# Performance work log

Hardware: AMD Instinct MI355X
Metric: run time of the kernel (lower is better)

The kernel has to match this reference:

```python
import jax, jax.numpy as jnp
import numpy as np

B, F, C = 16384, 256, 256


def setup_inputs() -> dict:
    key = jax.random.key(0)
    ks = jax.random.split(key, 10)
    return {
        "x_t": jax.random.normal(ks[0], (B, F), dtype=jnp.float32),
        "n_t": jax.random.normal(ks[1], (B, C), dtype=jnp.float32),
        "d_t": jax.random.uniform(ks[2], (B, C), dtype=jnp.float32),
        "h_t": jax.random.normal(ks[3], (B, C), dtype=jnp.float32),
        "a_max_t": jax.random.normal(ks[4], (B, C), dtype=jnp.float32),
        "Wu": jax.random.normal(ks[5], (C, F), dtype=jnp.float32) * 0.06,
        "bu": jnp.zeros((C,), dtype=jnp.float32),
        "Wg": jax.random.normal(ks[6], (C, F + C), dtype=jnp.float32) * 0.05,
        "bg": jnp.zeros((C,), dtype=jnp.float32),
        "Wa": jax.random.normal(ks[7], (C, F + C), dtype=jnp.float32) * 0.05,
        "Wd": jax.random.normal(ks[8], (C, F + C), dtype=jnp.float32) * 0.05,
    }


def reference(x_t, n_t, d_t, h_t, a_max_t, Wu, bu, Wg, bg, Wa, Wd):
    # xh_join = cat([x_t, h_t], dim=1) -> [B, F+C]
    xh = jnp.concatenate([x_t, h_t], axis=1)
    u_t = x_t @ Wu.T + bu                      # [B, C]
    g_t = xh @ Wg.T + bg                       # [B, C]
    a_t = xh @ Wa.T                            # [B, C] (no bias)
    z_t = u_t * jnp.tanh(g_t)
    # decay branch (self.decay is an nn.Linear -> always truthy in original)
    decay = jax.nn.sigmoid(xh @ Wd.T)
    e_neg = jnp.exp(-decay)
    a_decay = a_max_t * e_neg
    a_newmax = jnp.maximum(a_decay, a_t)
    exp_diff = jnp.exp(a_max_t - a_newmax)
    exp_scaled = jnp.exp(a_t - a_newmax)
    n_new = n_t * e_neg * exp_diff + z_t * exp_scaled
    d_new = d_t * e_neg * exp_diff + exp_scaled
    h_new = jnp.tanh(n_new / d_new)
    return (n_new, d_new, h_new, a_newmax)
```

## Files before the change

### kernel.cpp

```cpp
#include <hip/hip_runtime.h>
#include <stdint.h>

typedef _Float16 f16x8 __attribute__((ext_vector_type(8)));
typedef __fp16 fp16x2 __attribute__((ext_vector_type(2)));
typedef float f32x4 __attribute__((ext_vector_type(4)));

#define BC (16384 * 256)

__device__ __forceinline__ f16x8 cvt8(f32x4 a, f32x4 b) {
  fp16x2 p0 = __builtin_amdgcn_cvt_pkrtz(a[0], a[1]);
  fp16x2 p1 = __builtin_amdgcn_cvt_pkrtz(a[2], a[3]);
  fp16x2 p2 = __builtin_amdgcn_cvt_pkrtz(b[0], b[1]);
  fp16x2 p3 = __builtin_amdgcn_cvt_pkrtz(b[2], b[3]);
  f16x8 o;
  o[0] = (_Float16)p0[0]; o[1] = (_Float16)p0[1];
  o[2] = (_Float16)p1[0]; o[3] = (_Float16)p1[1];
  o[4] = (_Float16)p2[0]; o[5] = (_Float16)p2[1];
  o[6] = (_Float16)p3[0]; o[7] = (_Float16)p3[1];
  return o;
}

__device__ __forceinline__ float tanh_fast(float v) {
  float a = fminf(fabsf(v), 18.f);
  float t = __expf(2.f * a);
  float r = (t - 1.f) * __builtin_amdgcn_rcpf(t + 1.f);
  return copysignf(r, v);
}

__global__ __launch_bounds__(256) void pack_w(const float* __restrict__ Wu,
                                              const float* __restrict__ Wg,
                                              const float* __restrict__ Wa,
                                              const float* __restrict__ Wd,
                                              _Float16* __restrict__ wsB) {
  int t = blockIdx.x * 256 + threadIdx.x;
  int slot = t & 7;
  int kt = (t >> 3) & 7;
  int row = (t >> 6) & 127;
  int cb = t >> 13;
  int strip = (row >> 4) & 3;
  int wn = row >> 6;
  int t16 = row & 15;
  int c = cb * 32 + wn * 16 + t16;
  int k0 = kt * 64 + (slot ^ (row & 7)) * 8;
  float v[8];
  if (strip == 0) {
    if (k0 < 256) {
      const float* p = Wu + (size_t)c * 256 + k0;
#pragma unroll
      for (int i = 0; i < 8; ++i) v[i] = p[i];
    } else {
#pragma unroll
      for (int i = 0; i < 8; ++i) v[i] = 0.f;
    }
  } else {
    const float* p = (strip == 1 ? Wg : (strip == 2 ? Wa : Wd)) + (size_t)c * 512 + k0;
#pragma unroll
    for (int i = 0; i < 8; ++i) v[i] = p[i];
  }
  f32x4 a = {v[0], v[1], v[2], v[3]};
  f32x4 b = {v[4], v[5], v[6], v[7]};
  *reinterpret_cast<f16x8*>(wsB + (size_t)cb * 65536 + row * 512 + kt * 64 + slot * 8) =
      cvt8(a, b);
}

__global__ __launch_bounds__(256, 6) void rwa_main(
    const float* __restrict__ x, const float* __restrict__ nt_,
    const float* __restrict__ dt_, const float* __restrict__ h,
    const float* __restrict__ amax_, const float* __restrict__ bu,
    const float* __restrict__ bg, const _Float16* __restrict__ wsB,
    float* __restrict__ out) {
  __shared__ __align__(16) _Float16 ldsA[64 * 64];
  __shared__ __align__(16) _Float16 ldsB[128 * 64];

  const int tid = threadIdx.x;
  const int lane = tid & 63;
  const int l15 = lane & 15;
  const int lg = lane >> 4;
  const int wv = tid >> 6;
  const int wm = wv & 1;
  const int wn = wv >> 1;

  const int bid = blockIdx.x;
  const int xcd = bid & 7;
  const int q = bid >> 3;
  const int cb = q & 7;
  const int rowblk = xcd * 32 + (q >> 3);
  const int row0 = rowblk * 64;

  const int ar = tid >> 2;
  const int aq = tid & 3;

  const _Float16* bsrc0 = wsB + (size_t)cb * 65536 + (tid >> 3) * 512 + (tid & 7) * 8;

  f32x4 acc[2][4] = {};

  for (int kt = 0; kt < 8; ++kt) {
#pragma unroll
    for (int i = 0; i < 4; ++i) {
      __builtin_amdgcn_global_load_lds(
          (const __attribute__((address_space(1))) uint32_t*)(bsrc0 + i * 16384 + kt * 64),
          (__attribute__((address_space(3))) uint32_t*)(ldsB + wv * 512 + i * 2048),
          16, 0, 0);
    }
    {
      const float* asrc =
          (kt < 4 ? x : h) + (size_t)(row0 + ar) * 256 + (kt & 3) * 64 + aq * 16;
      f32x4 av[4];
#pragma unroll
      for (int i = 0; i < 4; ++i) av[i] = *reinterpret_cast<const f32x4*>(asrc + i * 4);
#pragma unroll
      for (int j = 0; j < 2; ++j) {
        f16x8 o = cvt8(av[2 * j], av[2 * j + 1]);
        const int slot = (aq * 2 + j) ^ (ar & 7);
        *reinterpret_cast<f16x8*>(reinterpret_cast<char*>(ldsA) + ar * 128 + slot * 16) = o;
      }
    }
    __syncthreads();

    const bool doU = (kt < 4);
    const int rswz = (l15 & 7) << 4;
#pragma unroll
    for (int ks = 0; ks < 2; ++ks) {
      f16x8 af[2], bf[4];
#pragma unroll
      for (int mi = 0; mi < 2; ++mi) {
        const int row = wm * 32 + mi * 16 + l15;
        af[mi] = *reinterpret_cast<const f16x8*>(
            reinterpret_cast<const char*>(ldsA) + row * 128 + ((ks * 64 + lg * 16) ^ rswz));
      }
#pragma unroll
      for (int s = 0; s < 4; ++s) {
        if (s == 0 && !doU) continue;
        const int row = wn * 64 + s * 16 + l15;
        bf[s] = *reinterpret_cast<const f16x8*>(
            reinterpret_cast<const char*>(ldsB) + row * 128 + ((ks * 64 + lg * 16) ^ rswz));
      }
#pragma unroll
      for (int s = 0; s < 4; ++s) {
        if (s == 0 && !doU) continue;
#pragma unroll
        for (int mi = 0; mi < 2; ++mi)
          acc[mi][s] = __builtin_amdgcn_mfma_f32_16x16x32_f16(af[mi], bf[s], acc[mi][s], 0, 0, 0);
      }
    }
    __syncthreads();
  }

  const int c = cb * 32 + wn * 16 + l15;
  const float buv = bu[c];
  const float bgv = bg[c];
#pragma unroll
  for (int mi = 0; mi < 2; ++mi) {
#pragma unroll
    for (int rg = 0; rg < 4; ++rg) {
      const int r = row0 + wm * 32 + mi * 16 + lg * 4 + rg;
      const int idx = r * 256 + c;
      const float u = acc[mi][0][rg] + buv;
      const float gt = acc[mi][1][rg] + bgv;
      const float a = acc[mi][2][rg];
      const float dr = acc[mi][3][rg];
      const float sig = __builtin_amdgcn_rcpf(1.f + __expf(-dr));
      const float z = u * tanh_fast(gt);
      const float am = amax_[idx];
      const float e_neg = __expf(-sig);
      const float a_new = fmaxf(am * e_neg, a);
      const float comm = __expf(am - a_new - sig);
      const float escal = __expf(a - a_new);
      const float n_new = nt_[idx] * comm + z * escal;
      const float d_new = dt_[idx] * comm + escal;
      const float h_new = tanh_fast(n_new * __builtin_amdgcn_rcpf(d_new));
      out[idx] = n_new;
      out[BC + idx] = d_new;
      out[2 * BC + idx] = h_new;
      out[3 * BC + idx] = a_new;
    }
  }
}

extern "C" void kernel_launch(void* const* d_in, const int* in_sizes, int n_in,
                              void* d_out, int out_size, void* d_ws, size_t ws_size,
                              hipStream_t stream) {
  const float* x_t    = (const float*)d_in[0];
  const float* n_t    = (const float*)d_in[1];
  const float* d_t    = (const float*)d_in[2];
  const float* h_t    = (const float*)d_in[3];
  const float* amax_t = (const float*)d_in[4];
  const float* Wu     = (const float*)d_in[5];
  const float* bu     = (const float*)d_in[6];
  const float* Wg     = (const float*)d_in[7];
  const float* bg     = (const float*)d_in[8];
  const float* Wa     = (const float*)d_in[9];
  const float* Wd     = (const float*)d_in[10];
  float* out = (float*)d_out;

  _Float16* wsB = (_Float16*)d_ws;

  pack_w<<<256, 256, 0, stream>>>(Wu, Wg, Wa, Wd, wsB);
  rwa_main<<<2048, 256, 0, stream>>>(x_t, n_t, d_t, h_t, amax_t, bu, bg, wsB, out);
}
```

Baseline: 52.65 us.

## Pre-pack activations into MFMA fragment layout and stream GEMM without LDS

Adds a pack_a kernel that converts x and h to fp16 in MFMA fragment order in workspace, and repacks weights in fragment order too. A new rwa_stream kernel then loads A and B fragments straight from global memory into registers, with no LDS staging or barriers. Each wave computes 32 rows by 32 columns. This removes LDS traffic and synchronisation, at the cost of an extra 16MB fp16 write and read pass over the activations and one more kernel launch. The old LDS path is kept as a fallback when the workspace is too small.

```diff
diff --git a/kernel.cpp b/kernel.cpp
--- a/kernel.cpp
+++ b/kernel.cpp
@@ -27,11 +27,138 @@
   return copysignf(r, v);
 }
 
-__global__ __launch_bounds__(256) void pack_w(const float* __restrict__ Wu,
-                                              const float* __restrict__ Wg,
-                                              const float* __restrict__ Wa,
-                                              const float* __restrict__ Wd,
-                                              _Float16* __restrict__ wsB) {
+
+__global__ __launch_bounds__(256) void pack_w_frag(const float* __restrict__ Wu,
+                                                   const float* __restrict__ Wg,
+                                                   const float* __restrict__ Wa,
+                                                   const float* __restrict__ Wd,
+                                                   _Float16* __restrict__ wsB) {
+  int tid = blockIdx.x * 256 + threadIdx.x;
+  int lg = tid & 3;
+  int l15 = (tid >> 2) & 15;
+  int f = (tid >> 6) & 7;
+  int w = (tid >> 9) & 7;
+  int kc = tid >> 12;
+  int s = f & 3;
+  int g = f >> 2;
+  int c = w * 32 + g * 16 + l15;
+  int k0 = kc * 32 + lg * 8;
+  float v[8];
+  if (s == 0) {
+    if (k0 < 256) {
+      const float* p = Wu + (size_t)c * 256 + k0;
+#pragma unroll
+      for (int i = 0; i < 8; ++i) v[i] = p[i];
+    } else {
+#pragma unroll
+      for (int i = 0; i < 8; ++i) v[i] = 0.f;
+    }
+  } else {
+    const float* p = (s == 1 ? Wg : (s == 2 ? Wa : Wd)) + (size_t)c * 512 + k0;
+#pragma unroll
+    for (int i = 0; i < 8; ++i) v[i] = p[i];
+  }
+  f32x4 a = {v[0], v[1], v[2], v[3]};
+  f32x4 b = {v[4], v[5], v[6], v[7]};
+  *reinterpret_cast<f16x8*>(wsB + (size_t)tid * 8) = cvt8(a, b);
+}
+
+__global__ __launch_bounds__(256) void pack_a(const float* __restrict__ x,
+                                              const float* __restrict__ h,
+                                              _Float16* __restrict__ wsA) {
+  int tid = blockIdx.x * 256 + threadIdx.x;
+  int l15 = tid & 15;
+  int lg = (tid >> 4) & 3;
+  int kc = (tid >> 6) & 15;
+  int row16 = tid >> 10;
+  int row = row16 * 16 + l15;
+  const float* src = (kc < 8)
+      ? (x + (size_t)row * 256 + kc * 32 + lg * 8)
+      : (h + (size_t)row * 256 + (kc - 8) * 32 + lg * 8);
+  f32x4 a = *reinterpret_cast<const f32x4*>(src);
+  f32x4 b = *reinterpret_cast<const f32x4*>(src + 4);
+  *reinterpret_cast<f16x8*>(wsA + (size_t)tid * 8) = cvt8(a, b);
+}
+
+__global__ __launch_bounds__(256, 4) void rwa_stream(
+    const float* __restrict__ nt_, const float* __restrict__ dt_,
+    const float* __restrict__ amax_, const float* __restrict__ bu,
+    const float* __restrict__ bg, const _Float16* __restrict__ wsA,
+    const _Float16* __restrict__ wsB, float* __restrict__ out) {
+  const int tid = threadIdx.x;
+  const int lane = tid & 63;
+  const int l15 = lane & 15;
+  const int lg = lane >> 4;
+  const int wv = tid >> 6;
+  const int bid = blockIdx.x;
+  const int cb = bid & 7;
+  const int w32 = (bid >> 3) * 4 + wv;
+  const int row0 = w32 * 32;
+
+  const _Float16* aa = wsA + (size_t)(w32 * 2) * 8192 + (size_t)lane * 8;
+  const _Float16* bb = wsB + (size_t)cb * 4096 + (size_t)(l15 * 4 + lg) * 8;
+
+  f32x4 acc[2][2][4] = {};
+
+#pragma unroll
+  for (int kc = 0; kc < 16; ++kc) {
+    f16x8 af0 = *reinterpret_cast<const f16x8*>(aa + kc * 512);
+    f16x8 af1 = *reinterpret_cast<const f16x8*>(aa + 8192 + kc * 512);
+    const _Float16* bk = bb + (size_t)kc * 32768;
+#pragma unroll
+    for (int g = 0; g < 2; ++g) {
+#pragma unroll
+      for (int s = 0; s < 4; ++s) {
+        if (s == 0 && kc >= 8) continue;
+        f16x8 bf = *reinterpret_cast<const f16x8*>(bk + (g * 4 + s) * 512);
+        acc[0][g][s] =
+            __builtin_amdgcn_mfma_f32_16x16x32_f16(af0, bf, acc[0][g][s], 0, 0, 0);
+        acc[1][g][s] =
+            __builtin_amdgcn_mfma_f32_16x16x32_f16(af1, bf, acc[1][g][s], 0, 0, 0);
+      }
+    }
+  }
+
+#pragma unroll
+  for (int g = 0; g < 2; ++g) {
+    const int c = cb * 32 + g * 16 + l15;
+    const float buv = bu[c];
+    const float bgv = bg[c];
+#pragma unroll
+    for (int mi = 0; mi < 2; ++mi) {
+#pragma unroll
+      for (int rg = 0; rg < 4; ++rg) {
+        const int r = row0 + mi * 16 + lg * 4 + rg;
+        const int idx = r * 256 + c;
+        const float u = acc[mi][g][0][rg] + buv;
+        const float gt = acc[mi][g][1][rg] + bgv;
+        const float a = acc[mi][g][2][rg];
+        const float dr = acc[mi][g][3][rg];
+        const float sig = __builtin_amdgcn_rcpf(1.f + __expf(-dr));
+        const float z = u * tanh_fast(gt);
+        const float am = amax_[idx];
+        const float e_neg = __expf(-sig);
+        const float a_new = fmaxf(am * e_neg, a);
+        const float comm = __expf(am - a_new - sig);
+        const float escal = __expf(a - a_new);
+        const float n_new = nt_[idx] * comm + z * escal;
+        const float d_new = dt_[idx] * comm + escal;
+        const float h_new = tanh_fast(n_new * __builtin_amdgcn_rcpf(d_new));
+        out[idx] = n_new;
+        out[BC + idx] = d_new;
+        out[2 * BC + idx] = h_new;
+        out[3 * BC + idx] = a_new;
+      }
+    }
+  }
+}
+
+
+__global__ __launch_bounds__(256) void pack_w_swz(const float* __restrict__ Wu,
+                                                  const float* __restrict__ Wg,
+                                                  const float* __restrict__ Wa,
+                                                  const float* __restrict__ Wd,
+                                                  _Float16* __restrict__ wsB) {
   int t = blockIdx.x * 256 + threadIdx.x;
   int slot = t & 7;
   int kt = (t >> 3) & 7;
@@ -63,7 +190,7 @@
       cvt8(a, b);
 }
 
-__global__ __launch_bounds__(256, 6) void rwa_main(
+__global__ __launch_bounds__(256, 6) void rwa_lds(
     const float* __restrict__ x, const float* __restrict__ nt_,
     const float* __restrict__ dt_, const float* __restrict__ h,
     const float* __restrict__ amax_, const float* __restrict__ bu,
@@ -193,8 +320,16 @@
   const float* Wd     = (const float*)d_in[10];
   float* out = (float*)d_out;
 
-  _Float16* wsB = (_Float16*)d_ws;
-
-  pack_w<<<256, 256, 0, stream>>>(Wu, Wg, Wa, Wd, wsB);
-  rwa_main<<<2048, 256, 0, stream>>>(x_t, n_t, d_t, h_t, amax_t, bu, bg, wsB, out);
-}
+  const size_t NEED = (size_t)1048576 + (size_t)16777216;
+  if (ws_size >= NEED) {
+    _Float16* wsB = (_Float16*)d_ws;
+    _Float16* wsA = (_Float16*)((char*)d_ws + 1048576);
+    pack_w_frag<<<256, 256, 0, stream>>>(Wu, Wg, Wa, Wd, wsB);
+    pack_a<<<4096, 256, 0, stream>>>(x_t, h_t, wsA);
+    rwa_stream<<<1024, 256, 0, stream>>>(n_t, d_t, amax_t, bu, bg, wsA, wsB, out);
+  } else {
+    _Float16* wsB = (_Float16*)d_ws;
+    pack_w_swz<<<256, 256, 0, stream>>>(Wu, Wg, Wa, Wd, wsB);
+    rwa_lds<<<2048, 256, 0, stream>>>(x_t, n_t, d_t, h_t, amax_t, bu, bg, wsB, out);
+  }
+}
```

New measurement: 76.59 us. 1.45x slower.

## Double-buffer K loop with 32-wide tiles and nontemporal epilogue memory ops

Applied to the files above, without the earlier changes.

The main GEMM loop now uses 16 K-steps of 32 instead of 8 of 64, with ping-pong LDS buffers for A and B. The next tile's global loads are issued before the current tile's MFMAs, and one barrier per step replaces two. The weight pack kernel is relaid out to match the new tile order with a contiguous store. Epilogue loads and stores become nontemporal to reduce cache pollution, in exchange for more loop iterations and extra register pressure from the prefetched A values.

```diff
diff --git a/kernel.cpp b/kernel.cpp
--- a/kernel.cpp
+++ b/kernel.cpp
@@ -32,16 +32,16 @@
                                               const float* __restrict__ Wa,
                                               const float* __restrict__ Wd,
                                               _Float16* __restrict__ wsB) {
-  int t = blockIdx.x * 256 + threadIdx.x;
-  int slot = t & 7;
-  int kt = (t >> 3) & 7;
-  int row = (t >> 6) & 127;
-  int cb = t >> 13;
+  int tid = blockIdx.x * 256 + threadIdx.x;
+  int slot = tid & 3;
+  int row = (tid >> 2) & 127;
+  int cb = (tid >> 9) & 7;
+  int kt = tid >> 12;
   int strip = (row >> 4) & 3;
   int wn = row >> 6;
   int t16 = row & 15;
   int c = cb * 32 + wn * 16 + t16;
-  int k0 = kt * 64 + (slot ^ (row & 7)) * 8;
+  int k0 = kt * 32 + (slot ^ ((row >> 1) & 3)) * 8;
   float v[8];
   if (strip == 0) {
     if (k0 < 256) {
@@ -59,8 +59,7 @@
   }
   f32x4 a = {v[0], v[1], v[2], v[3]};
   f32x4 b = {v[4], v[5], v[6], v[7]};
-  *reinterpret_cast<f16x8*>(wsB + (size_t)cb * 65536 + row * 512 + kt * 64 + slot * 8) =
-      cvt8(a, b);
+  *reinterpret_cast<f16x8*>(wsB + (size_t)tid * 8) = cvt8(a, b);
 }
 
 __global__ __launch_bounds__(256, 6) void rwa_main(
@@ -69,8 +68,8 @@
     const float* __restrict__ amax_, const float* __restrict__ bu,
     const float* __restrict__ bg, const _Float16* __restrict__ wsB,
     float* __restrict__ out) {
-  __shared__ __align__(16) _Float16 ldsA[64 * 64];
-  __shared__ __align__(16) _Float16 ldsB[128 * 64];
+  __shared__ __align__(16) _Float16 ldsA[2][64 * 32];
+  __shared__ __align__(16) _Float16 ldsB[2][128 * 32];
 
   const int tid = threadIdx.x;
   const int lane = tid & 63;
@@ -89,51 +88,59 @@
 
   const int ar = tid >> 2;
   const int aq = tid & 3;
-
-  const _Float16* bsrc0 = wsB + (size_t)cb * 65536 + (tid >> 3) * 512 + (tid & 7) * 8;
+  const int awoff = ar * 64 + ((aq ^ ((ar >> 1) & 3)) << 4);
+
+  const _Float16* bsrc0 = wsB + (size_t)cb * 4096 + (size_t)tid * 8;
 
   f32x4 acc[2][4] = {};
-
-  for (int kt = 0; kt < 8; ++kt) {
-#pragma unroll
-    for (int i = 0; i < 4; ++i) {
+  f32x4 a0, a1;
+
+  auto issueA = [&](int kt) {
+    const float* sp = (kt < 8 ? x : h) + (size_t)(row0 + ar) * 256 + (kt & 7) * 32 + aq * 8;
+    a0 = *reinterpret_cast<const f32x4*>(sp);
+    a1 = *reinterpret_cast<const f32x4*>(sp + 4);
+  };
+  auto issueB = [&](int buf, int kt) {
+#pragma unroll
+    for (int i = 0; i < 2; ++i) {
       __builtin_amdgcn_global_load_lds(
-          (const __attribute__((address_space(1))) uint32_t*)(bsrc0 + i * 16384 + kt * 64),
-          (__attribute__((address_space(3))) uint32_t*)(ldsB + wv * 512 + i * 2048),
+          (const __attribute__((address_space(1))) uint32_t*)(bsrc0 + (size_t)kt * 32768 + i * 2048),
+          (__attribute__((address_space(3))) uint32_t*)(&ldsB[buf][0]) + tid * 4 + i * 1024,
           16, 0, 0);
     }
+  };
+  auto writeA = [&](int buf) {
+    *reinterpret_cast<f16x8*>(reinterpret_cast<char*>(&ldsA[buf][0]) + awoff) = cvt8(a0, a1);
+  };
+
+  issueA(0);
+  issueB(0, 0);
+  writeA(0);
+  __syncthreads();
+
+#pragma unroll
+  for (int kt = 0; kt < 16; ++kt) {
+    const int buf = kt & 1;
+    if (kt < 15) {
+      issueA(kt + 1);
+      issueB(buf ^ 1, kt + 1);
+    }
+
+    const bool doU = (kt < 8);
     {
-      const float* asrc =
-          (kt < 4 ? x : h) + (size_t)(row0 + ar) * 256 + (kt & 3) * 64 + aq * 16;
-      f32x4 av[4];
-#pragma unroll
-      for (int i = 0; i < 4; ++i) av[i] = *reinterpret_cast<const f32x4*>(asrc + i * 4);
-#pragma unroll
-      for (int j = 0; j < 2; ++j) {
-        f16x8 o = cvt8(av[2 * j], av[2 * j + 1]);
-        const int slot = (aq * 2 + j) ^ (ar & 7);
-        *reinterpret_cast<f16x8*>(reinterpret_cast<char*>(ldsA) + ar * 128 + slot * 16) = o;
-      }
-    }
-    __syncthreads();
-
-    const bool doU = (kt < 4);
-    const int rswz = (l15 & 7) << 4;
-#pragma unroll
-    for (int ks = 0; ks < 2; ++ks) {
+      const char* pA = reinterpret_cast<const char*>(&ldsA[buf][0]);
+      const char* pB = reinterpret_cast<const char*>(&ldsB[buf][0]);
       f16x8 af[2], bf[4];
 #pragma unroll
       for (int mi = 0; mi < 2; ++mi) {
         const int row = wm * 32 + mi * 16 + l15;
-        af[mi] = *reinterpret_cast<const f16x8*>(
-            reinterpret_cast<const char*>(ldsA) + row * 128 + ((ks * 64 + lg * 16) ^ rswz));
+        af[mi] = *reinterpret_cast<const f16x8*>(pA + row * 64 + ((lg ^ ((row >> 1) & 3)) << 4));
       }
 #pragma unroll
       for (int s = 0; s < 4; ++s) {
         if (s == 0 && !doU) continue;
-        const int row = wn * 64 + s * 16 + l15;
-        bf[s] = *reinterpret_cast<const f16x8*>(
-            reinterpret_cast<const char*>(ldsB) + row * 128 + ((ks * 64 + lg * 16) ^ rswz));
+        const int pc = wn * 64 + s * 16 + l15;
+        bf[s] = *reinterpret_cast<const f16x8*>(pB + pc * 64 + ((lg ^ ((pc >> 1) & 3)) << 4));
       }
 #pragma unroll
       for (int s = 0; s < 4; ++s) {
@@ -143,7 +150,11 @@
           acc[mi][s] = __builtin_amdgcn_mfma_f32_16x16x32_f16(af[mi], bf[s], acc[mi][s], 0, 0, 0);
       }
     }
-    __syncthreads();
+
+    if (kt < 15) {
+      writeA(buf ^ 1);
+      __syncthreads();
+    }
   }
 
   const int c = cb * 32 + wn * 16 + l15;
@@ -161,18 +172,20 @@
       const float dr = acc[mi][3][rg];
       const float sig = __builtin_amdgcn_rcpf(1.f + __expf(-dr));
       const float z = u * tanh_fast(gt);
-      const float am = amax_[idx];
+      const float am = __builtin_nontemporal_load(amax_ + idx);
+      const float n_old = __builtin_nontemporal_load(nt_ + idx);
+      const float d_old = __builtin_nontemporal_load(dt_ + idx);
       const float e_neg = __expf(-sig);
       const float a_new = fmaxf(am * e_neg, a);
       const float comm = __expf(am - a_new - sig);
       const float escal = __expf(a - a_new);
-      const float n_new = nt_[idx] * comm + z * escal;
-      const float d_new = dt_[idx] * comm + escal;
+      const float n_new = n_old * comm + z * escal;
+      const float d_new = d_old * comm + escal;
       const float h_new = tanh_fast(n_new * __builtin_amdgcn_rcpf(d_new));
-      out[idx] = n_new;
-      out[BC + idx] = d_new;
-      out[2 * BC + idx] = h_new;
-      out[3 * BC + idx] = a_new;
+      __builtin_nontemporal_store(n_new, out + idx);
+      __builtin_nontemporal_store(d_new, out + BC + idx);
+      __builtin_nontemporal_store(h_new, out + 2 * BC + idx);
+      __builtin_nontemporal_store(a_new, out + 3 * BC + idx);
     }
   }
 }
```

Result: slower. 76.66 us (+45.6%).

## Double-buffer LDS tiles to prefetch next K-slice during MFMA compute

Applied to the files above, without the earlier changes.

Splits the A and B shared-memory tiles into two buffers so the next K-step's global loads (A into registers, B via direct-to-LDS loads) are issued before the current step's MFMAs, and one barrier per iteration is removed. This is meant to hide global load latency behind compute. In exchange it doubles LDS use to 48KB per block and lowers the occupancy hint from 6 to 3 blocks per CU, which reduces latency hiding across waves. The epilogue also hoists the n_t/d_t loads earlier.

```diff
diff --git a/kernel.cpp b/kernel.cpp
--- a/kernel.cpp
+++ b/kernel.cpp
@@ -63,14 +63,14 @@
       cvt8(a, b);
 }
 
-__global__ __launch_bounds__(256, 6) void rwa_main(
+__global__ __launch_bounds__(256, 3) void rwa_main(
     const float* __restrict__ x, const float* __restrict__ nt_,
     const float* __restrict__ dt_, const float* __restrict__ h,
     const float* __restrict__ amax_, const float* __restrict__ bu,
     const float* __restrict__ bg, const _Float16* __restrict__ wsB,
     float* __restrict__ out) {
-  __shared__ __align__(16) _Float16 ldsA[64 * 64];
-  __shared__ __align__(16) _Float16 ldsB[128 * 64];
+  __shared__ __align__(16) _Float16 ldsA[2][64 * 64];
+  __shared__ __align__(16) _Float16 ldsB[2][128 * 64];
 
   const int tid = threadIdx.x;
   const int lane = tid & 63;
@@ -93,31 +93,47 @@
   const _Float16* bsrc0 = wsB + (size_t)cb * 65536 + (tid >> 3) * 512 + (tid & 7) * 8;
 
   f32x4 acc[2][4] = {};
-
-  for (int kt = 0; kt < 8; ++kt) {
+  f32x4 av[4];
+
+  auto issueA = [&](int kt) {
+    const float* sp = (kt < 4 ? x : h) + (size_t)(row0 + ar) * 256 + (kt & 3) * 64 + aq * 16;
+#pragma unroll
+    for (int i = 0; i < 4; ++i) av[i] = *reinterpret_cast<const f32x4*>(sp + i * 4);
+  };
+  auto issueB = [&](int buf, int kt) {
 #pragma unroll
     for (int i = 0; i < 4; ++i) {
       __builtin_amdgcn_global_load_lds(
-          (const __attribute__((address_space(1))) uint32_t*)(bsrc0 + i * 16384 + kt * 64),
-          (__attribute__((address_space(3))) uint32_t*)(ldsB + wv * 512 + i * 2048),
+          (const __attribute__((address_space(1))) uint32_t*)(bsrc0 + (size_t)kt * 64 + i * 16384),
+          (__attribute__((address_space(3))) uint32_t*)(&ldsB[buf][0] + wv * 512 + i * 2048),
           16, 0, 0);
     }
-    {
-      const float* asrc =
-          (kt < 4 ? x : h) + (size_t)(row0 + ar) * 256 + (kt & 3) * 64 + aq * 16;
-      f32x4 av[4];
-#pragma unroll
-      for (int i = 0; i < 4; ++i) av[i] = *reinterpret_cast<const f32x4*>(asrc + i * 4);
-#pragma unroll
-      for (int j = 0; j < 2; ++j) {
-        f16x8 o = cvt8(av[2 * j], av[2 * j + 1]);
-        const int slot = (aq * 2 + j) ^ (ar & 7);
-        *reinterpret_cast<f16x8*>(reinterpret_cast<char*>(ldsA) + ar * 128 + slot * 16) = o;
-      }
-    }
-    __syncthreads();
+  };
+  auto writeA = [&](int buf) {
+#pragma unroll
+    for (int j = 0; j < 2; ++j) {
+      f16x8 o = cvt8(av[2 * j], av[2 * j + 1]);
+      const int slot = (aq * 2 + j) ^ (ar & 7);
+      *reinterpret_cast<f16x8*>(reinterpret_cast<char*>(&ldsA[buf][0]) + ar * 128 + slot * 16) = o;
+    }
+  };
+
+  issueA(0);
+  issueB(0, 0);
+  writeA(0);
+  __syncthreads();
+
+#pragma unroll
+  for (int kt = 0; kt < 8; ++kt) {
+    const int buf = kt & 1;
+    if (kt < 7) {
+      issueA(kt + 1);
+      issueB(buf ^ 1, kt + 1);
+    }
 
     const bool doU = (kt < 4);
+    const char* pA = reinterpret_cast<const char*>(&ldsA[buf][0]);
+    const char* pB = reinterpret_cast<const char*>(&ldsB[buf][0]);
     const int rswz = (l15 & 7) << 4;
 #pragma unroll
     for (int ks = 0; ks < 2; ++ks) {
@@ -125,15 +141,13 @@
 #pragma unroll
       for (int mi = 0; mi < 2; ++mi) {
         const int row = wm * 32 + mi * 16 + l15;
-        af[mi] = *reinterpret_cast<const f16x8*>(
-            reinterpret_cast<const char*>(ldsA) + row * 128 + ((ks * 64 + lg * 16) ^ rswz));
+        af[mi] = *reinterpret_cast<const f16x8*>(pA + row * 128 + ((ks * 64 + lg * 16) ^ rswz));
       }
 #pragma unroll
       for (int s = 0; s < 4; ++s) {
         if (s == 0 && !doU) continue;
-        const int row = wn * 64 + s * 16 + l15;
-        bf[s] = *reinterpret_cast<const f16x8*>(
-            reinterpret_cast<const char*>(ldsB) + row * 128 + ((ks * 64 + lg * 16) ^ rswz));
+        const int pc = wn * 64 + s * 16 + l15;
+        bf[s] = *reinterpret_cast<const f16x8*>(pB + pc * 128 + ((ks * 64 + lg * 16) ^ rswz));
       }
 #pragma unroll
       for (int s = 0; s < 4; ++s) {
@@ -143,7 +157,11 @@
           acc[mi][s] = __builtin_amdgcn_mfma_f32_16x16x32_f16(af[mi], bf[s], acc[mi][s], 0, 0, 0);
       }
     }
-    __syncthreads();
+
+    if (kt < 7) {
+      writeA(buf ^ 1);
+      __syncthreads();
+    }
   }
 
   const int c = cb * 32 + wn * 16 + l15;
@@ -162,12 +180,14 @@
       const float sig = __builtin_amdgcn_rcpf(1.f + __expf(-dr));
       const float z = u * tanh_fast(gt);
       const float am = amax_[idx];
+      const float n_old = nt_[idx];
+      const float d_old = dt_[idx];
       const float e_neg = __expf(-sig);
       const float a_new = fmaxf(am * e_neg, a);
       const float comm = __expf(am - a_new - sig);
       const float escal = __expf(a - a_new);
-      const float n_new = nt_[idx] * comm + z * escal;
-      const float d_new = dt_[idx] * comm + escal;
+      const float n_new = n_old * comm + z * escal;
+      const float d_new = d_old * comm + escal;
       const float h_new = tanh_fast(n_new * __builtin_amdgcn_rcpf(d_new));
       out[idx] = n_new;
       out[BC + idx] = d_new;
```

New measurement: 52.88 us. No clear change (+0.4%).
